# Performance work log

Hardware: AMD Instinct MI355X
Metric: run time of the kernel (lower is better)

The kernel has to match this reference:

```python
import jax, jax.numpy as jnp
import numpy as np

K = 3  # kernel size, stride=1, padding=0 (hardcoded in SingleAdder)


def setup_inputs() -> dict:
    key = jax.random.key(0)
    x = jax.random.normal(key, (16, 5, 512, 512), dtype=jnp.float32)
    # adder weight is initialized to all-ones in SingleAdder.__init__
    W = jnp.ones((5, 5, 3, 3), dtype=jnp.float32)
    return {"x": x, "W": W}


def adder2d(x, W):
    """AdderNet conv: out[n,co,i,j] = -sum_{ci,kh,kw} |x[n,ci,i+kh,j+kw] - W[co,ci,kh,kw]|.
    Loop over the 9 fixed kernel taps (not data dims); each tap is fully vectorized.
    Avoids materializing a full im2col tensor."""
    B, Ci, H, Wd = x.shape
    Co = W.shape[0]
    Ho, Wo = H - K + 1, Wd - K + 1
    out = jnp.zeros((B, Co, Ho, Wo), dtype=x.dtype)
    for kh in range(K):
        for kw in range(K):
            patch = x[:, None, :, kh:kh + Ho, kw:kw + Wo]        # [B,1,Ci,Ho,Wo]
            w = W[None, :, :, kh, kw, None, None]                # [1,Co,Ci,1,1]
            out = out - jnp.sum(jnp.abs(patch - w), axis=2)      # reduce over Ci
    return out


def reference(x, W):
    return adder2d(x, W)
```

## Files before the change

### kernel.cpp

```cpp
#include <hip/hip_runtime.h>


#define KK 3
#define NB 16
#define CI 5
#define CO 5
#define H 512
#define WD 512
#define HO 510
#define WO 510
#define TW 64
#define TH 16

__global__ __launch_bounds__(256)
void adder2d_kernel(const float* __restrict__ x,
                    const float* __restrict__ Wg,
                    float* __restrict__ out) {
    const int tx = threadIdx.x & 63;
    const int ty = threadIdx.x >> 6;
    const int j0 = blockIdx.x * TW;
    const int i0 = blockIdx.y * TH;
    const int n  = blockIdx.z;

    const int j     = j0 + tx;
    const int ibase = i0 + ty * 4;

    float xv[CI][6][KK];
    const float* xn = x + (size_t)n * CI * H * WD;
    #pragma unroll
    for (int ci = 0; ci < CI; ++ci) {
        #pragma unroll
        for (int r = 0; r < 6; ++r) {
            int gi = ibase + r;
            gi = gi < H ? gi : H - 1;
            const float* rowp = xn + (size_t)ci * H * WD + (size_t)gi * WD;
            #pragma unroll
            for (int k = 0; k < KK; ++k) {
                int gj = j + k;
                gj = gj < WD ? gj : WD - 1;
                xv[ci][r][k] = rowp[gj];
            }
        }
    }

    const bool jvalid = (j < WO);
    float* outn = out + (size_t)n * CO * HO * WO;

    #pragma unroll 1
    for (int co = 0; co < CO; ++co) {
        float acc0 = 0.f, acc1 = 0.f, acc2 = 0.f, acc3 = 0.f;
        const float* wp = Wg + co * (CI * KK * KK);
        #pragma unroll
        for (int ci = 0; ci < CI; ++ci) {
            #pragma unroll
            for (int kh = 0; kh < KK; ++kh) {
                #pragma unroll
                for (int kw = 0; kw < KK; ++kw) {
                    const float w = wp[ci * 9 + kh * 3 + kw];
                    acc0 += fabsf(xv[ci][kh + 0][kw] - w);
                    acc1 += fabsf(xv[ci][kh + 1][kw] - w);
                    acc2 += fabsf(xv[ci][kh + 2][kw] - w);
                    acc3 += fabsf(xv[ci][kh + 3][kw] - w);
                }
            }
        }
        if (jvalid) {
            float accs[4] = {acc0, acc1, acc2, acc3};
            float* outc = outn + (size_t)co * HO * WO;
            #pragma unroll
            for (int rr = 0; rr < 4; ++rr) {
                const int i = ibase + rr;
                if (i < HO) outc[(size_t)i * WO + j] = -accs[rr];
            }
        }
    }
}

extern "C" void kernel_launch(void* const* d_in, const int* in_sizes, int n_in,
                              void* d_out, int out_size, void* d_ws, size_t ws_size,
                              hipStream_t stream) {
    const float* x  = (const float*)d_in[0];
    const float* Wg = (const float*)d_in[1];
    float* out      = (float*)d_out;

    dim3 grid((WO + TW - 1) / TW,
              (HO + TH - 1) / TH,
              NB);
    dim3 block(256);
    adder2d_kernel<<<grid, block, 0, stream>>>(x, Wg, out);
}
```

Baseline: 158.0 us.

## Interchange channel loops to stream inputs per channel with all-output accumulators

The input-channel loop becomes the outer loop. Each iteration loads only a 6x3 window for that channel and updates 20 accumulators covering all 5 output channels times 4 rows. Before, all 90 input values for every channel were held in registers while looping over output channels. The change aims to cut register pressure, which may raise occupancy, and it drops per-load column clamping by clamping the column once. In exchange it keeps more accumulators live, makes the channel loop non-unrolled, and issues all output stores at the end.

```diff
diff --git a/kernel.cpp b/kernel.cpp
--- a/kernel.cpp
+++ b/kernel.cpp
@@ -25,52 +25,67 @@
     const int j     = j0 + tx;
     const int ibase = i0 + ty * 4;
 
-    float xv[CI][6][KK];
-    const float* xn = x + (size_t)n * CI * H * WD;
+    const int jc = j < WO ? j : (WO - 1);
+    int rowoff[6];
     #pragma unroll
+    for (int r = 0; r < 6; ++r) {
+        int gi = ibase + r;
+        gi = gi < H ? gi : (H - 1);
+        rowoff[r] = gi * WD;
+    }
+
+    const float* xn = x + (size_t)n * CI * H * WD + jc;
+
+    float acc[CO][4];
+    #pragma unroll
+    for (int co = 0; co < CO; ++co)
+        #pragma unroll
+        for (int r = 0; r < 4; ++r) acc[co][r] = 0.f;
+
+    #pragma unroll 1
     for (int ci = 0; ci < CI; ++ci) {
+        const float* p = xn + (size_t)ci * H * WD;
+        float xw[6][KK];
         #pragma unroll
         for (int r = 0; r < 6; ++r) {
-            int gi = ibase + r;
-            gi = gi < H ? gi : H - 1;
-            const float* rowp = xn + (size_t)ci * H * WD + (size_t)gi * WD;
+            const float* rp = p + rowoff[r];
+            xw[r][0] = rp[0];
+            xw[r][1] = rp[1];
+            xw[r][2] = rp[2];
+        }
+        const float* wp = Wg + ci * (KK * KK);
+        #pragma unroll
+        for (int kh = 0; kh < KK; ++kh) {
             #pragma unroll
-            for (int k = 0; k < KK; ++k) {
-                int gj = j + k;
-                gj = gj < WD ? gj : WD - 1;
-                xv[ci][r][k] = rowp[gj];
+            for (int kw = 0; kw < KK; ++kw) {
+                const int widx = kh * KK + kw;
+                float w0 = wp[0 * 45 + widx];
+                float w1 = wp[1 * 45 + widx];
+                float w2 = wp[2 * 45 + widx];
+                float w3 = wp[3 * 45 + widx];
+                float w4 = wp[4 * 45 + widx];
+                #pragma unroll
+                for (int r = 0; r < 4; ++r) {
+                    const float xv = xw[kh + r][kw];
+                    acc[0][r] += fabsf(xv - w0);
+                    acc[1][r] += fabsf(xv - w1);
+                    acc[2][r] += fabsf(xv - w2);
+                    acc[3][r] += fabsf(xv - w3);
+                    acc[4][r] += fabsf(xv - w4);
+                }
             }
         }
     }
 
-    const bool jvalid = (j < WO);
-    float* outn = out + (size_t)n * CO * HO * WO;
-
-    #pragma unroll 1
-    for (int co = 0; co < CO; ++co) {
-        float acc0 = 0.f, acc1 = 0.f, acc2 = 0.f, acc3 = 0.f;
-        const float* wp = Wg + co * (CI * KK * KK);
+    if (j < WO) {
+        float* outn = out + (size_t)n * CO * HO * WO;
         #pragma unroll
-        for (int ci = 0; ci < CI; ++ci) {
-            #pragma unroll
-            for (int kh = 0; kh < KK; ++kh) {
-                #pragma unroll
-                for (int kw = 0; kw < KK; ++kw) {
-                    const float w = wp[ci * 9 + kh * 3 + kw];
-                    acc0 += fabsf(xv[ci][kh + 0][kw] - w);
-                    acc1 += fabsf(xv[ci][kh + 1][kw] - w);
-                    acc2 += fabsf(xv[ci][kh + 2][kw] - w);
-                    acc3 += fabsf(xv[ci][kh + 3][kw] - w);
-                }
-            }
-        }
-        if (jvalid) {
-            float accs[4] = {acc0, acc1, acc2, acc3};
+        for (int co = 0; co < CO; ++co) {
             float* outc = outn + (size_t)co * HO * WO;
             #pragma unroll
-            for (int rr = 0; rr < 4; ++rr) {
-                const int i = ibase + rr;
-                if (i < HO) outc[(size_t)i * WO + j] = -accs[rr];
+            for (int r = 0; r < 4; ++r) {
+                const int i = ibase + r;
+                if (i < HO) outc[(size_t)i * WO + j] = -acc[co][r];
             }
         }
     }
```

After: 166.7 us. +5.5%, slower.
